# Optimization experiments

Hardware: AMD Instinct MI355X
Metric: run time of the kernel (lower is better)

The kernel has to match this reference:

```python
import jax, jax.numpy as jnp
import numpy as np

B, P, E = 256, 196, 2048           # batch, num_pixels, encoder_size
H, A, EMB = 2048, 512, 300         # hidden, attention, embedding dims
V_IN, V_OUT = 262, 261             # input vocab (classes+2), output (classes+1)
T = 7                              # max_seq_len + 2


def setup_inputs() -> dict:
    key = jax.random.key(0)
    ks = jax.random.split(key, 20)
    s = 0.02
    return {
        "encoder_feature_out": jax.random.normal(ks[0], (B, P, E), jnp.float32),
        "encoder_out": jax.random.normal(ks[1], (B, E), jnp.float32),
        "annotations_X": jax.random.randint(ks[2], (B, T), 0, V_IN),
        "is_train": 1,
        "emb_W": jax.random.normal(ks[3], (V_IN, EMB), jnp.float32) * s,
        "feat_W": jax.random.normal(ks[4], (H, E), jnp.float32) * s,
        "feat_b": jnp.zeros((H,), jnp.float32),
        "W_ih": jax.random.normal(ks[5], (4 * H, EMB + E), jnp.float32) * s,
        "W_hh": jax.random.normal(ks[6], (4 * H, H), jnp.float32) * s,
        "b_ih": jnp.zeros((4 * H,), jnp.float32),
        "b_hh": jnp.zeros((4 * H,), jnp.float32),
        "enc_att_W": jax.random.normal(ks[7], (A, E), jnp.float32) * s,
        "enc_att_b": jnp.zeros((A,), jnp.float32),
        "dec_att_W": jax.random.normal(ks[8], (A, H), jnp.float32) * s,
        "dec_att_b": jnp.zeros((A,), jnp.float32),
        "full_att_W": jax.random.normal(ks[9], (1, A), jnp.float32) * s,
        "full_att_b": jnp.zeros((1,), jnp.float32),
        "fbeta_W": jax.random.normal(ks[10], (E, H), jnp.float32) * s,
        "fbeta_b": jnp.zeros((E,), jnp.float32),
        "fc_W": jax.random.normal(ks[11], (V_OUT, H), jnp.float32) * s,
        "fc_b": jnp.zeros((V_OUT,), jnp.float32),
    }


def _forward(encoder_feature_out, encoder_out, annotations_X,
             emb_W, feat_W, feat_b, W_ih, W_hh, b_ih, b_hh,
             enc_att_W, enc_att_b, dec_att_W, dec_att_b,
             full_att_W, full_att_b, fbeta_W, fbeta_b, fc_W, fc_b):
    enc = encoder_feature_out                                  # (B,P,E)
    # encoder side of additive attention is constant across steps
    att1 = jnp.einsum('bpe,ae->bpa', enc, enc_att_W) + enc_att_b  # (B,P,A)
    h0 = encoder_out @ feat_W.T + feat_b                       # (B,H)
    c0 = jnp.zeros_like(h0)

    def step(carry, ann_t):
        h, c = carry
        # additive attention
        att2 = h @ dec_att_W.T + dec_att_b                     # (B,A)
        e = jax.nn.relu(att1 + att2[:, None, :]) @ full_att_W[0] + full_att_b[0]  # (B,P)
        alpha = jax.nn.softmax(e, axis=1)                      # (B,P)
        awe = jnp.einsum('bp,bpe->be', alpha, enc)             # (B,E)
        gate = jax.nn.sigmoid(h @ fbeta_W.T + fbeta_b)         # (B,E)
        awe = gate * awe
        # LSTMCell (dropout layers in eval mode -> identity)
        x = jnp.concatenate([emb_W[ann_t], awe], axis=1)       # (B,EMB+E)
        gates = x @ W_ih.T + b_ih + h @ W_hh.T + b_hh          # (B,4H)
        i, f, g, o = jnp.split(gates, 4, axis=1)
        c = jax.nn.sigmoid(f) * c + jax.nn.sigmoid(i) * jnp.tanh(g)
        h = jax.nn.sigmoid(o) * jnp.tanh(c)
        yhat = h @ fc_W.T + fc_b                               # (B,V_OUT)
        return (h, c), (yhat, alpha)

    _, (yhats, alphas) = jax.lax.scan(step, (h0, c0), annotations_X.T)  # (T,B,...)
    return jnp.transpose(yhats, (1, 0, 2)), jnp.transpose(alphas, (1, 0, 2))


def reference(encoder_feature_out, encoder_out, annotations_X, is_train,
              emb_W, feat_W, feat_b, W_ih, W_hh, b_ih, b_hh,
              enc_att_W, enc_att_b, dec_att_W, dec_att_b,
              full_att_W, full_att_b, fbeta_W, fbeta_b, fc_W, fc_b):
    # is_train=True (teacher forcing) path
    return _forward(encoder_feature_out, encoder_out, annotations_X,
                    emb_W, feat_W, feat_b, W_ih, W_hh, b_ih, b_hh,
                    enc_att_W, enc_att_b, dec_att_W, dec_att_b,
                    full_att_W, full_att_b, fbeta_W, fbeta_b, fc_W, fc_b)
```

## Files before the change

kernel.cpp:

```cpp
#include <hip/hip_runtime.h>
#include <math.h>

#define B_    256
#define P_    196
#define E_    2048
#define H_    2048
#define A_    512
#define EMB_  300
#define VOUT_ 261
#define T_    7

#define KPAD_   4608
#define EMBOFF_ 2048
#define AWEOFF_ 2352

#define NSTEP_  2880
#define FCOFF_  2560
#define GSPLIT_ 8
#define PSPLIT_ 4
#define PCHUNK_ 49

typedef __attribute__((ext_vector_type(8))) short          short8_t;
typedef __attribute__((ext_vector_type(8))) unsigned short ushort8_t;
typedef __attribute__((ext_vector_type(4))) float          f32x4;

__device__ __forceinline__ unsigned short f2b(float f) {
    union { float f; unsigned int u; } v; v.f = f;
    unsigned int x = v.u;
    unsigned int r = (x + 0x7fffu + ((x >> 16) & 1u)) >> 16;
    return (unsigned short)r;
}
__device__ __forceinline__ float b2f(unsigned short u) {
    union { unsigned int u; float f; } v; v.u = ((unsigned int)u) << 16;
    return v.f;
}
__device__ __forceinline__ ushort8_t pack8(float4 u0, float4 u1) {
    ushort8_t u;
    u[0]=f2b(u0.x); u[1]=f2b(u0.y); u[2]=f2b(u0.z); u[3]=f2b(u0.w);
    u[4]=f2b(u1.x); u[5]=f2b(u1.y); u[6]=f2b(u1.z); u[7]=f2b(u1.w);
    return u;
}

template<bool SPLITK, bool OUT16, bool XCDSWZ>
__global__ __launch_bounds__(256)
void gemm_sk(const unsigned short* __restrict__ Ab, int lda,
             const unsigned short* __restrict__ Bw, int ldb,
             void* __restrict__ Cout, int ldc,
             int Kper, int colbase, const float* __restrict__ bias, int nbx)
{
    __shared__ ushort8_t As8[256 * 8];
    __shared__ ushort8_t Bs8[64 * 8];

    const int tid  = threadIdx.x;
    const int lane = tid & 63;
    const int w    = tid >> 6;

    int nblk, mblk;
    if (XCDSWZ) {
        const int bid  = blockIdx.x;
        const int pair = (bid & 7) * (gridDim.x >> 3) + (bid >> 3);
        nblk = pair % nbx;
        mblk = pair / nbx;
    } else {
        nblk = blockIdx.x;
        mblk = 0;
    }
    const int col0  = colbase + nblk * 64;
    const int kbase = SPLITK ? blockIdx.y * Kper : 0;
    const int mrow0 = XCDSWZ ? mblk * 256 : 0;

    const int rb  = tid >> 3;
    const int seg = tid & 7;
    const int swz = seg ^ (rb & 7);

    const unsigned short* Ap = Ab + (size_t)(mrow0 + rb) * lda + kbase + seg * 8;
    const unsigned short* Bp = Bw + (size_t)(col0 + rb) * ldb + kbase + seg * 8;

    const int lr = lane & 15;
    const int hi = lane >> 4;

    f32x4 acc[4][4];
    #pragma unroll
    for (int m = 0; m < 4; ++m)
        #pragma unroll
        for (int n = 0; n < 4; ++n)
            acc[m][n] = (f32x4){0.f, 0.f, 0.f, 0.f};

    ushort8_t aR[8], bR[2];
    #pragma unroll
    for (int i = 0; i < 8; ++i)
        aR[i] = *(const ushort8_t*)(Ap + (size_t)i * 32 * lda);
    bR[0] = *(const ushort8_t*)(Bp);
    bR[1] = *(const ushort8_t*)(Bp + (size_t)32 * ldb);

    for (int k0 = 0; k0 < Kper; k0 += 64) {
        __syncthreads();
        #pragma unroll
        for (int i = 0; i < 8; ++i)
            As8[(rb + i * 32) * 8 + swz] = aR[i];
        Bs8[rb * 8 + swz]        = bR[0];
        Bs8[(rb + 32) * 8 + swz] = bR[1];
        __syncthreads();
        if (k0 + 64 < Kper) {
            #pragma unroll
            for (int i = 0; i < 8; ++i)
                aR[i] = *(const ushort8_t*)(Ap + (size_t)i * 32 * lda + k0 + 64);
            bR[0] = *(const ushort8_t*)(Bp + k0 + 64);
            bR[1] = *(const ushort8_t*)(Bp + (size_t)32 * ldb + k0 + 64);
        }
        #pragma unroll
        for (int kc = 0; kc < 2; ++kc) {
            short8_t af[4], bf[4];
            #pragma unroll
            for (int m = 0; m < 4; ++m) {
                const int row = w * 64 + m * 16 + lr;
                af[m] = *(const short8_t*)&As8[row * 8 + ((kc * 4 + hi) ^ (row & 7))];
            }
            #pragma unroll
            for (int n = 0; n < 4; ++n) {
                const int row = n * 16 + lr;
                bf[n] = *(const short8_t*)&Bs8[row * 8 + ((kc * 4 + hi) ^ (row & 7))];
            }
            #pragma unroll
            for (int m = 0; m < 4; ++m)
                #pragma unroll
                for (int n = 0; n < 4; ++n)
                    acc[m][n] = __builtin_amdgcn_mfma_f32_16x16x32_bf16(
                        af[m], bf[n], acc[m][n], 0, 0, 0);
        }
    }

    if (OUT16) {
        unsigned short* C16 = (unsigned short*)Cout;
        #pragma unroll
        for (int m = 0; m < 4; ++m) {
            const int grow0 = mrow0 + w * 64 + m * 16 + hi * 4;
            #pragma unroll
            for (int n = 0; n < 4; ++n) {
                const int gcol = col0 + n * 16 + lr;
                const float bv = bias[gcol];
                #pragma unroll
                for (int r = 0; r < 4; ++r)
                    C16[(size_t)(grow0 + r) * ldc + gcol] = f2b(acc[m][n][r] + bv);
            }
        }
    } else {
        float* Cs = (float*)Cout + (SPLITK ? (size_t)blockIdx.y * 256 * ldc : 0);
        #pragma unroll
        for (int m = 0; m < 4; ++m) {
            const int grow0 = w * 64 + m * 16 + hi * 4;
            #pragma unroll
            for (int n = 0; n < 4; ++n) {
                const int gcol = col0 + n * 16 + lr;
                #pragma unroll
                for (int r = 0; r < 4; ++r)
                    Cs[(size_t)(grow0 + r) * ldc + gcol] = acc[m][n][r];
            }
        }
    }
}

__global__ __launch_bounds__(256)
void gemm_mfma_f32(const float* __restrict__ Af, int lda,
                   const unsigned short* __restrict__ Bw, int ldb,
                   unsigned short* __restrict__ Cp, int ldc,
                   const float* __restrict__ bias,
                   int M, int N, int K)
{
    __shared__ __align__(16) unsigned short As[64][40];
    __shared__ __align__(16) unsigned short Bs[128][40];

    const int tid  = threadIdx.x;
    const int lane = tid & 63;
    const int wid  = tid >> 6;
    const int wr   = wid >> 1;
    const int wc   = wid & 1;
    const int row0 = blockIdx.y * 64;
    const int col0 = blockIdx.x * 128;

    const int ar = tid >> 2;
    const int as = (tid & 3) * 8;
    const int br = tid >> 1;
    const int bs = (tid & 1) * 16;

    const int lr = lane & 15;
    const int lk = (lane >> 4) * 8;

    f32x4 acc[2][4];
    #pragma unroll
    for (int m = 0; m < 2; ++m)
        #pragma unroll
        for (int n = 0; n < 4; ++n)
            acc[m][n] = (f32x4){0.f, 0.f, 0.f, 0.f};

    for (int k0 = 0; k0 < K; k0 += 32) {
        ushort8_t aval = {0,0,0,0,0,0,0,0};
        if (row0 + ar < M) {
            const float* p = Af + (size_t)(row0 + ar) * lda + k0 + as;
            aval = pack8(*(const float4*)(p), *(const float4*)(p + 4));
        }
        ushort8_t bv0 = {0,0,0,0,0,0,0,0}, bv1 = {0,0,0,0,0,0,0,0};
        if (col0 + br < N) {
            const unsigned short* p = Bw + (size_t)(col0 + br) * ldb + k0 + bs;
            bv0 = *(const ushort8_t*)(p);
            bv1 = *(const ushort8_t*)(p + 8);
        }
        __syncthreads();
        *(ushort8_t*)&As[ar][as]     = aval;
        *(ushort8_t*)&Bs[br][bs]     = bv0;
        *(ushort8_t*)&Bs[br][bs + 8] = bv1;
        __syncthreads();

        short8_t af[2], bf[4];
        #pragma unroll
        for (int m = 0; m < 2; ++m)
            af[m] = *(const short8_t*)&As[wr * 32 + m * 16 + lr][lk];
        #pragma unroll
        for (int n = 0; n < 4; ++n)
            bf[n] = *(const short8_t*)&Bs[wc * 64 + n * 16 + lr][lk];
        #pragma unroll
        for (int m = 0; m < 2; ++m)
            #pragma unroll
            for (int n = 0; n < 4; ++n)
                acc[m][n] = __builtin_amdgcn_mfma_f32_16x16x32_bf16(
                    af[m], bf[n], acc[m][n], 0, 0, 0);
    }

    #pragma unroll
    for (int m = 0; m < 2; ++m) {
        const int grow0 = row0 + wr * 32 + m * 16 + (lane >> 4) * 4;
        #pragma unroll
        for (int n = 0; n < 4; ++n) {
            const int gcol = col0 + wc * 64 + n * 16 + lr;
            if (gcol >= N) continue;
            const float bv = bias[gcol];
            #pragma unroll
            for (int r = 0; r < 4; ++r) {
                const int grow = grow0 + r;
                if (grow >= M) continue;
                Cp[(size_t)grow * ldc + gcol] = f2b(acc[m][n][r] + bv);
            }
        }
    }
}

__global__ __launch_bounds__(256)
void cvt_bf16_kernel(const float* __restrict__ in, unsigned short* __restrict__ out,
                     int n8)
{
    const int idx = blockIdx.x * 256 + threadIdx.x;
    if (idx >= n8) return;
    const size_t base = (size_t)idx * 8;
    *(ushort8_t*)(out + base) =
        pack8(*(const float4*)(in + base), *(const float4*)(in + base + 4));
}

__global__ __launch_bounds__(256)
void setup_kernel(const float* __restrict__ b_ih, const float* __restrict__ b_hh,
                  float* __restrict__ bias4h,
                  const float* __restrict__ enc_attW, unsigned short* __restrict__ encattW16,
                  const float* __restrict__ feat_W, unsigned short* __restrict__ featW16,
                  const float* __restrict__ enc_out, unsigned short* __restrict__ encout16,
                  const float* __restrict__ dec_attW, const float* __restrict__ fbeta_W,
                  const float* __restrict__ fc_W, unsigned short* __restrict__ wstep,
                  unsigned short* __restrict__ xcat, float* __restrict__ cbuf)
{
    int bid = blockIdx.x;
    const int tid = threadIdx.x;
    if (bid < 32) {
        const int i = bid * 256 + tid;
        bias4h[i] = b_ih[i] + b_hh[i];
        return;
    }
    bid -= 32;
    if (bid < 512) {
        const size_t base = ((size_t)bid * 256 + tid) * 8;
        *(ushort8_t*)(encattW16 + base) =
            pack8(*(const float4*)(enc_attW + base), *(const float4*)(enc_attW + base + 4));
        return;
    }
    bid -= 512;
    if (bid < 2048) {
        const size_t base = ((size_t)bid * 256 + tid) * 8;
        *(ushort8_t*)(featW16 + base) =
            pack8(*(const float4*)(feat_W + base), *(const float4*)(feat_W + base + 4));
        return;
    }
    bid -= 2048;
    if (bid < 256) {
        const size_t base = ((size_t)bid * 256 + tid) * 8;
        *(ushort8_t*)(encout16 + base) =
            pack8(*(const float4*)(enc_out + base), *(const float4*)(enc_out + base + 4));
        return;
    }
    bid -= 256;
    if (bid < NSTEP_) {
        const int row = bid;
        const int c0  = tid * 8;
        const float* src;
        if (row < A_)                   src = dec_attW + (size_t)row * H_ + c0;
        else if (row < A_ + E_)         src = fbeta_W + (size_t)(row - A_) * H_ + c0;
        else if (row < A_ + E_ + VOUT_) src = fc_W + (size_t)(row - A_ - E_) * H_ + c0;
        else                            src = nullptr;
        ushort8_t u = {0,0,0,0,0,0,0,0};
        if (src) u = pack8(*(const float4*)(src), *(const float4*)(src + 4));
        *(ushort8_t*)(wstep + (size_t)row * H_ + c0) = u;
        return;
    }
    bid -= NSTEP_;
    if (bid < 576) {
        const size_t base = ((size_t)bid * 256 + tid) * 8;
        ushort8_t z = {0,0,0,0,0,0,0,0};
        *(ushort8_t*)(xcat + base) = z;
        return;
    }
    bid -= 576;
    {
        const size_t base = ((size_t)bid * 256 + tid) * 4;
        *(float4*)(cbuf + base) = make_float4(0.f, 0.f, 0.f, 0.f);
    }
}

__global__ __launch_bounds__(256)
void build_wcat_kernel(const float* __restrict__ W_ih, const float* __restrict__ W_hh,
                       unsigned short* __restrict__ wcat)
{
    const int row = blockIdx.x;
    const int LIH = EMB_ + E_;
    for (int s = threadIdx.x; s < KPAD_ / 8; s += 256) {
        const int k0 = s * 8;
        ushort8_t u;
        const float* src = nullptr;
        if (k0 + 8 <= H_)                         src = W_hh + (size_t)row * H_ + k0;
        else if (k0 >= H_ && k0 + 8 <= 2344)      src = W_ih + (size_t)row * LIH + (k0 - H_);
        else if (k0 >= AWEOFF_ && k0 + 8 <= 4400) src = W_ih + (size_t)row * LIH + (k0 - 2052);
        if (src) {
            u = pack8(*(const float4*)(src), *(const float4*)(src + 4));
        } else {
            #pragma unroll
            for (int i = 0; i < 8; ++i) {
                const int k = k0 + i;
                float v = 0.f;
                if (k >= H_ && k < 2348)           v = W_ih[(size_t)row * LIH + (k - H_)];
                else if (k >= AWEOFF_ && k < 4400) v = W_ih[(size_t)row * LIH + (k - 2052)];
                u[i] = f2b(v);
            }
        }
        *(ushort8_t*)(wcat + (size_t)row * KPAD_ + k0) = u;
    }
}

__global__ __launch_bounds__(256)
void reduce_h0(const float* __restrict__ parts, const float* __restrict__ bias,
               unsigned short* __restrict__ xcat)
{
    const int i = blockIdx.x * 256 + threadIdx.x;
    const int row = i >> 11, col = i & (H_ - 1);
    float acc = bias[col];
    #pragma unroll
    for (int s = 0; s < 8; ++s)
        acc += parts[(size_t)s * 256 * H_ + i];
    xcat[(size_t)row * KPAD_ + col] = f2b(acc);
}

__global__ __launch_bounds__(256)
void att_awe_kernel(const float* __restrict__ parts, const float* __restrict__ dec_attb,
                    const unsigned short* __restrict__ att1,
                    const float* __restrict__ fw_g, const float* __restrict__ fb,
                    const float* __restrict__ encf, const unsigned short* __restrict__ enc16,
                    int use16,
                    float* __restrict__ awe_part, float* __restrict__ out_a, int t)
{
    const int ph = blockIdx.x;
    const int b  = blockIdx.y;
    const int tid = threadIdx.x;
    const int lane = tid & 63;
    const int wid  = tid >> 6;
    __shared__ float att2s[A_];
    __shared__ float es[P_];
    __shared__ float red[4];

    #pragma unroll
    for (int it = 0; it < A_ / 256; ++it) {
        const int c = tid + it * 256;
        float acc = dec_attb[c];
        #pragma unroll
        for (int s = 0; s < 8; ++s)
            acc += parts[((size_t)s * B_ + b) * NSTEP_ + c];
        att2s[c] = acc;
    }
    __syncthreads();

    const int l32  = lane & 31;
    const int slot = wid * 2 + (lane >> 5);
    float a2r[16], fwr[16];
    #pragma unroll
    for (int k = 0; k < 16; ++k) {
        a2r[k] = att2s[l32 * 16 + k];
        fwr[k] = fw_g[l32 * 16 + k];
    }
    const float fbv = fb[0];

    for (int p = slot; p < P_; p += 8) {
        const unsigned short* row = att1 + ((size_t)b * P_ + p) * A_ + l32 * 16;
        ushort8_t v0 = *(const ushort8_t*)(row);
        ushort8_t v1 = *(const ushort8_t*)(row + 8);
        float acc = 0.f;
        #pragma unroll
        for (int k = 0; k < 8; ++k) {
            float x = b2f(v0[k]) + a2r[k];
            x = x > 0.f ? x : 0.f;
            acc = fmaf(x, fwr[k], acc);
        }
        #pragma unroll
        for (int k = 0; k < 8; ++k) {
            float x = b2f(v1[k]) + a2r[k + 8];
            x = x > 0.f ? x : 0.f;
            acc = fmaf(x, fwr[k + 8], acc);
        }
        #pragma unroll
        for (int off = 16; off > 0; off >>= 1)
            acc += __shfl_xor(acc, off);
        if (l32 == 0) es[p] = acc + fbv;
    }
    __syncthreads();

    float v = (tid < P_) ? es[tid] : -1e30f;
    float m = v;
    #pragma unroll
    for (int off = 32; off > 0; off >>= 1)
        m = fmaxf(m, __shfl_xor(m, off));
    if (lane == 0) red[wid] = m;
    __syncthreads();
    m = fmaxf(fmaxf(red[0], red[1]), fmaxf(red[2], red[3]));
    __syncthreads();
    float p = (tid < P_) ? expf(v - m) : 0.f;
    float s = p;
    #pragma unroll
    for (int off = 32; off > 0; off >>= 1)
        s += __shfl_xor(s, off);
    if (lane == 0) red[wid] = s;
    __syncthreads();
    s = red[0] + red[1] + red[2] + red[3];
    float alv = p / s;
    if (tid < P_) {
        if (ph == 0)
            out_a[((size_t)b * T_ + t) * P_ + tid] = alv;
    }
    __syncthreads();
    if (tid < P_) es[tid] = alv;
    __syncthreads();

    const int e0 = tid * 8;
    const int prow0 = ph * PCHUNK_;
    float acc[8] = {0.f,0.f,0.f,0.f,0.f,0.f,0.f,0.f};
    if (use16) {
        const unsigned short* ep = enc16 + ((size_t)b * P_ + prow0) * E_ + e0;
        int pp = 0;
        for (; pp + 4 <= PCHUNK_; pp += 4) {
            ushort8_t v0 = *(const ushort8_t*)(ep + (size_t)(pp + 0) * E_);
            ushort8_t v1 = *(const ushort8_t*)(ep + (size_t)(pp + 1) * E_);
            ushort8_t v2 = *(const ushort8_t*)(ep + (size_t)(pp + 2) * E_);
            ushort8_t v3 = *(const ushort8_t*)(ep + (size_t)(pp + 3) * E_);
            const float a0 = es[prow0 + pp],     a1 = es[prow0 + pp + 1];
            const float a2 = es[prow0 + pp + 2], a3 = es[prow0 + pp + 3];
            #pragma unroll
            for (int k = 0; k < 8; ++k) {
                float t0 = fmaf(a0, b2f(v0[k]), acc[k]);
                float t1 = fmaf(a1, b2f(v1[k]), t0);
                float t2 = fmaf(a2, b2f(v2[k]), t1);
                acc[k]   = fmaf(a3, b2f(v3[k]), t2);
            }
        }
        for (; pp < PCHUNK_; ++pp) {
            ushort8_t v0 = *(const ushort8_t*)(ep + (size_t)pp * E_);
            const float a0 = es[prow0 + pp];
            #pragma unroll
            for (int k = 0; k < 8; ++k)
                acc[k] = fmaf(a0, b2f(v0[k]), acc[k]);
        }
    } else {
        const float* ep = encf + ((size_t)b * P_ + prow0) * E_ + e0;
        for (int pp = 0; pp < PCHUNK_; ++pp) {
            float4 v0 = *(const float4*)(ep + (size_t)pp * E_);
            float4 v1 = *(const float4*)(ep + (size_t)pp * E_ + 4);
            const float a0 = es[prow0 + pp];
            acc[0] = fmaf(a0, v0.x, acc[0]); acc[1] = fmaf(a0, v0.y, acc[1]);
            acc[2] = fmaf(a0, v0.z, acc[2]); acc[3] = fmaf(a0, v0.w, acc[3]);
            acc[4] = fmaf(a0, v1.x, acc[4]); acc[5] = fmaf(a0, v1.y, acc[5]);
            acc[6] = fmaf(a0, v1.z, acc[6]); acc[7] = fmaf(a0, v1.w, acc[7]);
        }
    }
    float* dst = awe_part + ((size_t)ph * B_ + b) * E_ + e0;
    *(float4*)(dst)     = make_float4(acc[0], acc[1], acc[2], acc[3]);
    *(float4*)(dst + 4) = make_float4(acc[4], acc[5], acc[6], acc[7]);
}

__global__ __launch_bounds__(256)
void awe_fin_kernel(const float* __restrict__ parts, const float* __restrict__ fbeta_b,
                    const float* __restrict__ awe_part,
                    const int* __restrict__ ann, const float* __restrict__ embW,
                    unsigned short* __restrict__ xcat,
                    const float* __restrict__ fc_b, float* __restrict__ out_y, int t)
{
    const int b = blockIdx.x;
    const int tid = threadIdx.x;
    const int e0 = tid * 8;

    float aw[8] = {0.f,0.f,0.f,0.f,0.f,0.f,0.f,0.f};
    #pragma unroll
    for (int ph = 0; ph < PSPLIT_; ++ph) {
        float4 pa = *(const float4*)(awe_part + ((size_t)ph * B_ + b) * E_ + e0);
        float4 pb = *(const float4*)(awe_part + ((size_t)ph * B_ + b) * E_ + e0 + 4);
        aw[0] += pa.x; aw[1] += pa.y; aw[2] += pa.z; aw[3] += pa.w;
        aw[4] += pb.x; aw[5] += pb.y; aw[6] += pb.z; aw[7] += pb.w;
    }

    ushort8_t o;
    #pragma unroll
    for (int k = 0; k < 8; ++k) {
        float g = fbeta_b[e0 + k];
        #pragma unroll
        for (int s = 0; s < 8; ++s)
            g += parts[((size_t)s * B_ + b) * NSTEP_ + A_ + e0 + k];
        const float sg = 1.f / (1.f + expf(-g));
        o[k] = f2b(sg * aw[k]);
    }
    *(ushort8_t*)(xcat + (size_t)b * KPAD_ + AWEOFF_ + e0) = o;

    const int r = ann[b * T_ + t];
    for (int j = tid; j < EMB_; j += 256)
        xcat[(size_t)b * KPAD_ + EMBOFF_ + j] = f2b(embW[(size_t)r * EMB_ + j]);

    if (t > 0) {
        for (int c = tid; c < VOUT_; c += 256) {
            float a = fc_b[c];
            #pragma unroll
            for (int s = 0; s < 8; ++s)
                a += parts[((size_t)s * B_ + b) * NSTEP_ + FCOFF_ + c];
            out_y[((size_t)b * T_ + (t - 1)) * VOUT_ + c] = a;
        }
    }
}

__global__ __launch_bounds__(256)
void fc_reduce(const float* __restrict__ parts, const float* __restrict__ fc_b,
               float* __restrict__ out_y, int tm1)
{
    const int i = blockIdx.x * 256 + threadIdx.x;
    if (i >= B_ * VOUT_) return;
    const int b = i / VOUT_;
    const int c = i - b * VOUT_;
    float acc = fc_b[c];
    #pragma unroll
    for (int s = 0; s < 8; ++s)
        acc += parts[((size_t)s * B_ + b) * NSTEP_ + FCOFF_ + c];
    out_y[((size_t)b * T_ + tm1) * VOUT_ + c] = acc;
}

__global__ __launch_bounds__(256)
void lstm_kernel(const float* __restrict__ parts, const float* __restrict__ bias4h,
                 float* __restrict__ c, unsigned short* __restrict__ xcat)
{
    const int idx = blockIdx.x * 256 + threadIdx.x;
    const int b = idx >> 11;
    const int j = idx & (H_ - 1);
    const float* p0 = parts + (size_t)b * 4 * H_;
    const size_t S = (size_t)256 * 4 * H_;
    float gi = bias4h[j],          gf = bias4h[H_ + j];
    float gg = bias4h[2 * H_ + j], go = bias4h[3 * H_ + j];
    #pragma unroll
    for (int s = 0; s < GSPLIT_; ++s) {
        const float* p = p0 + s * S;
        gi += p[j]; gf += p[H_ + j]; gg += p[2 * H_ + j]; go += p[3 * H_ + j];
    }
    const float si = 1.f / (1.f + expf(-gi));
    const float sf = 1.f / (1.f + expf(-gf));
    const float so = 1.f / (1.f + expf(-go));
    const float cn = sf * c[idx] + si * tanhf(gg);
    c[idx] = cn;
    xcat[(size_t)b * KPAD_ + j] = f2b(so * tanhf(cn));
}

extern "C" void kernel_launch(void* const* d_in, const int* in_sizes, int n_in,
                              void* d_out, int out_size, void* d_ws, size_t ws_size,
                              hipStream_t stream)
{
    const float* enc      = (const float*)d_in[0];
    const float* enc_out  = (const float*)d_in[1];
    const int*   ann      = (const int*)  d_in[2];
    const float* emb_W    = (const float*)d_in[4];
    const float* feat_W   = (const float*)d_in[5];
    const float* feat_b   = (const float*)d_in[6];
    const float* W_ih     = (const float*)d_in[7];
    const float* W_hh     = (const float*)d_in[8];
    const float* b_ih     = (const float*)d_in[9];
    const float* b_hh     = (const float*)d_in[10];
    const float* enc_attW = (const float*)d_in[11];
    const float* enc_attb = (const float*)d_in[12];
    const float* dec_attW = (const float*)d_in[13];
    const float* dec_attb = (const float*)d_in[14];
    const float* full_attW= (const float*)d_in[15];
    const float* full_attb= (const float*)d_in[16];
    const float* fbeta_W  = (const float*)d_in[17];
    const float* fbeta_b  = (const float*)d_in[18];
    const float* fc_W     = (const float*)d_in[19];
    const float* fc_b     = (const float*)d_in[20];
    (void)in_sizes; (void)n_in; (void)out_size;

    float* out   = (float*)d_out;
    float* out_y = out;
    float* out_a = out + (size_t)B_ * T_ * VOUT_;

    char* base = (char*)d_ws;
    size_t off = 0;
    auto alloc = [&](size_t bytes) -> char* {
        char* p = base + off;
        off += (bytes + 255) & ~(size_t)255;
        return p;
    };
    unsigned short* att1_16   = (unsigned short*)alloc((size_t)B_ * P_ * A_ * 2);
    unsigned short* wcat16    = (unsigned short*)alloc((size_t)4 * H_ * KPAD_ * 2);
    unsigned short* wstep16   = (unsigned short*)alloc((size_t)NSTEP_ * H_ * 2);
    unsigned short* encattW16 = (unsigned short*)alloc((size_t)A_ * E_ * 2);
    unsigned short* featW16   = (unsigned short*)alloc((size_t)H_ * E_ * 2);
    unsigned short* encout16  = (unsigned short*)alloc((size_t)B_ * E_ * 2);
    unsigned short* xcat16    = (unsigned short*)alloc((size_t)B_ * KPAD_ * 2);
    float* cbuf     = (float*)alloc((size_t)B_ * H_ * 4);
    float* bias4h   = (float*)alloc((size_t)4 * H_ * 4);
    float* awe_part = (float*)alloc((size_t)PSPLIT_ * B_ * E_ * 4);
    const size_t parts_elems = (size_t)GSPLIT_ * B_ * 4 * H_;
    float* parts   = (float*)alloc(parts_elems * 4);
    const size_t enc_elems = (size_t)B_ * P_ * E_;
    const int use16 = (off + enc_elems * 2 <= ws_size) ? 1 : 0;
    unsigned short* enc16 = use16 ? (unsigned short*)alloc(enc_elems * 2) : nullptr;

    const dim3 blk(256);

    setup_kernel<<<dim3(32 + 512 + 2048 + 256 + NSTEP_ + 576 + 512), blk, 0, stream>>>(
        b_ih, b_hh, bias4h, enc_attW, encattW16, feat_W, featW16,
        enc_out, encout16, dec_attW, fbeta_W, fc_W, wstep16, xcat16, cbuf);
    build_wcat_kernel<<<dim3(4 * H_), blk, 0, stream>>>(W_ih, W_hh, wcat16);
    if (use16)
        cvt_bf16_kernel<<<dim3((int)(enc_elems / 8 + 255) / 256), blk, 0, stream>>>(
            enc, enc16, (int)(enc_elems / 8));

    if (use16) {
        gemm_sk<false, true, true><<<dim3(196 * 8), blk, 0, stream>>>(
            enc16, E_, encattW16, E_, att1_16, A_, E_, 0, enc_attb, 8);
    } else {
        dim3 g((A_ + 127) / 128, (B_ * P_) / 64);
        gemm_mfma_f32<<<g, blk, 0, stream>>>(enc, E_, encattW16, E_,
            att1_16, A_, enc_attb, B_ * P_, A_, E_);
    }
    gemm_sk<true, false, false><<<dim3(H_ / 64, 8), blk, 0, stream>>>(
        encout16, E_, featW16, E_, parts, H_, E_ / 8, 0, nullptr, 0);
    reduce_h0<<<dim3(B_ * H_ / 256), blk, 0, stream>>>(parts, feat_b, xcat16);

    for (int t = 0; t <= T_; ++t) {
        if (t < T_)
            gemm_sk<true, false, false><<<dim3(NSTEP_ / 64, 8), blk, 0, stream>>>(
                xcat16, KPAD_, wstep16, H_, parts, NSTEP_, H_ / 8, 0, nullptr, 0);
        else
            gemm_sk<true, false, false><<<dim3((NSTEP_ - FCOFF_) / 64, 8), blk, 0, stream>>>(
                xcat16, KPAD_, wstep16, H_, parts, NSTEP_, H_ / 8, FCOFF_, nullptr, 0);
        if (t == T_) {
            fc_reduce<<<dim3((B_ * VOUT_ + 255) / 256), blk, 0, stream>>>(parts, fc_b, out_y, t - 1);
            break;
        }

        att_awe_kernel<<<dim3(PSPLIT_, B_), blk, 0, stream>>>(
            parts, dec_attb, att1_16, full_attW, full_attb,
            enc, enc16, use16, awe_part, out_a, t);
        awe_fin_kernel<<<dim3(B_), blk, 0, stream>>>(parts, fbeta_b, awe_part,
                                                     ann, emb_W, xcat16, fc_b, out_y, t);

        gemm_sk<true, false, false><<<dim3(4 * H_ / 64, GSPLIT_), blk, 0, stream>>>(
            xcat16, KPAD_, wcat16, KPAD_, parts, 4 * H_, KPAD_ / GSPLIT_, 0, nullptr, 0);
        lstm_kernel<<<dim3(B_ * H_ / 256), blk, 0, stream>>>(parts, bias4h, cbuf, xcat16);
    }
}
```

Before: 1.371 ms.

## Load GEMM tiles directly into LDS and halve split-K/pixel-split factors

The GEMM kernel stops staging tiles through registers and instead uses global_load_lds to write 16-byte chunks straight into LDS, with the XOR swizzle moved onto the global source address. The register prefetch is dropped, so load and compute for a tile no longer overlap, and a second barrier is added per iteration. GSPLIT and PSPLIT are also halved (PCHUNK doubled), which cuts partial-sum traffic and reduction work but leaves fewer blocks per launch. The parts buffer is resized so it can also hold an 8-way split of the NSTEP weights.

New measurement: 1.261 ms. 1.09x faster.

```diff
diff --git a/kernel.cpp b/kernel.cpp
--- a/kernel.cpp
+++ b/kernel.cpp
@@ -16,9 +16,9 @@
 
 #define NSTEP_  2880
 #define FCOFF_  2560
-#define GSPLIT_ 8
-#define PSPLIT_ 4
-#define PCHUNK_ 49
+#define GSPLIT_ 4
+#define PSPLIT_ 2
+#define PCHUNK_ 98
 
 typedef __attribute__((ext_vector_type(8))) short          short8_t;
 typedef __attribute__((ext_vector_type(8))) unsigned short ushort8_t;
@@ -39,6 +39,13 @@
     u[0]=f2b(u0.x); u[1]=f2b(u0.y); u[2]=f2b(u0.z); u[3]=f2b(u0.w);
     u[4]=f2b(u1.x); u[5]=f2b(u1.y); u[6]=f2b(u1.z); u[7]=f2b(u1.w);
     return u;
+}
+
+__device__ __forceinline__ void gld_lds16(const unsigned short* g, const ushort8_t* l) {
+    __builtin_amdgcn_global_load_lds(
+        (const __attribute__((address_space(1))) void*)g,
+        (__attribute__((address_space(3))) void*)l,
+        16, 0, 0);
 }
 
 template<bool SPLITK, bool OUT16, bool XCDSWZ>
@@ -73,8 +80,8 @@
     const int seg = tid & 7;
     const int swz = seg ^ (rb & 7);
 
-    const unsigned short* Ap = Ab + (size_t)(mrow0 + rb) * lda + kbase + seg * 8;
-    const unsigned short* Bp = Bw + (size_t)(col0 + rb) * ldb + kbase + seg * 8;
+    const unsigned short* Ap = Ab + (size_t)(mrow0 + rb) * lda + kbase + swz * 8;
+    const unsigned short* Bp = Bw + (size_t)(col0 + rb) * ldb + kbase + swz * 8;
 
     const int lr = lane & 15;
     const int hi = lane >> 4;
@@ -86,28 +93,14 @@
         for (int n = 0; n < 4; ++n)
             acc[m][n] = (f32x4){0.f, 0.f, 0.f, 0.f};
 
-    ushort8_t aR[8], bR[2];
-    #pragma unroll
-    for (int i = 0; i < 8; ++i)
-        aR[i] = *(const ushort8_t*)(Ap + (size_t)i * 32 * lda);
-    bR[0] = *(const ushort8_t*)(Bp);
-    bR[1] = *(const ushort8_t*)(Bp + (size_t)32 * ldb);
-
     for (int k0 = 0; k0 < Kper; k0 += 64) {
+        #pragma unroll
+        for (int i = 0; i < 8; ++i)
+            gld_lds16(Ap + (size_t)i * 32 * lda + k0, &As8[(i * 32 + w * 8) * 8]);
+        gld_lds16(Bp + k0,                    &Bs8[(w * 8) * 8]);
+        gld_lds16(Bp + (size_t)32 * ldb + k0, &Bs8[(32 + w * 8) * 8]);
         __syncthreads();
-        #pragma unroll
-        for (int i = 0; i < 8; ++i)
-            As8[(rb + i * 32) * 8 + swz] = aR[i];
-        Bs8[rb * 8 + swz]        = bR[0];
-        Bs8[(rb + 32) * 8 + swz] = bR[1];
-        __syncthreads();
-        if (k0 + 64 < Kper) {
-            #pragma unroll
-            for (int i = 0; i < 8; ++i)
-                aR[i] = *(const ushort8_t*)(Ap + (size_t)i * 32 * lda + k0 + 64);
-            bR[0] = *(const ushort8_t*)(Bp + k0 + 64);
-            bR[1] = *(const ushort8_t*)(Bp + (size_t)32 * ldb + k0 + 64);
-        }
+
         #pragma unroll
         for (int kc = 0; kc < 2; ++kc) {
             short8_t af[4], bf[4];
@@ -128,6 +121,7 @@
                     acc[m][n] = __builtin_amdgcn_mfma_f32_16x16x32_bf16(
                         af[m], bf[n], acc[m][n], 0, 0, 0);
         }
+        __syncthreads();
     }
 
     if (OUT16) {
@@ -629,8 +623,9 @@
     float* cbuf     = (float*)alloc((size_t)B_ * H_ * 4);
     float* bias4h   = (float*)alloc((size_t)4 * H_ * 4);
     float* awe_part = (float*)alloc((size_t)PSPLIT_ * B_ * E_ * 4);
-    const size_t parts_elems = (size_t)GSPLIT_ * B_ * 4 * H_;
-    float* parts   = (float*)alloc(parts_elems * 4);
+    const size_t parts_elems = (size_t)8 * B_ * NSTEP_;
+    const size_t parts_elems2 = (size_t)GSPLIT_ * B_ * 4 * H_;
+    float* parts   = (float*)alloc((parts_elems > parts_elems2 ? parts_elems : parts_elems2) * 4);
     const size_t enc_elems = (size_t)B_ * P_ * E_;
     const int use16 = (off + enc_elems * 2 <= ws_size) ? 1 : 0;
     unsigned short* enc16 = use16 ? (unsigned short*)alloc(enc_elems * 2) : nullptr;
```
